# Kernel tuning notes

Hardware: AMD Instinct MI355X
Metric: run time of the kernel (lower is better)

The kernel has to match this reference:

```python
import jax, jax.numpy as jnp
import numpy as np

D_MODEL = 512
NHEAD = 8
D_K = D_MODEL // NHEAD


def setup_inputs() -> dict:
    key = jax.random.key(0)
    ks = jax.random.split(key, 7)
    B, L = 4, 2048
    x = jax.random.normal(ks[0], (B, L, D_MODEL), dtype=jnp.float32)
    scale = 1.0 / np.sqrt(D_MODEL)
    Wq = jax.random.normal(ks[1], (D_MODEL, D_MODEL), dtype=jnp.float32) * scale
    Wk = jax.random.normal(ks[2], (D_MODEL, D_MODEL), dtype=jnp.float32) * scale
    Wv = jax.random.normal(ks[3], (D_MODEL, D_MODEL), dtype=jnp.float32) * scale
    Wo = jax.random.normal(ks[4], (D_MODEL, D_MODEL), dtype=jnp.float32) * scale
    wave_freq = jax.random.normal(ks[5], (NHEAD,), dtype=jnp.float32) * 0.1
    wave_phase = jnp.zeros((NHEAD,), dtype=jnp.float32)
    return {"x": x, "Wq": Wq, "Wk": Wk, "Wv": Wv, "Wo": Wo,
            "wave_freq": wave_freq, "wave_phase": wave_phase}


def reference(x, Wq, Wk, Wv, Wo, wave_freq, wave_phase):
    B, L, D = x.shape
    H, dk = NHEAD, D_K
    # nn.Linear(bias=False): y = x @ W.T
    q = (x @ Wq.T).reshape(B, L, H, dk).transpose(0, 2, 1, 3)  # (B,H,L,dk)
    k = (x @ Wk.T).reshape(B, L, H, dk).transpose(0, 2, 1, 3)
    v = (x @ Wv.T).reshape(B, L, H, dk).transpose(0, 2, 1, 3)
    pos = jnp.arange(L, dtype=x.dtype)  # (L,)
    two_pi = jnp.asarray(2.0 * np.pi, dtype=x.dtype)
    # wave: (H, L) -> broadcast as (1, H, 1, L) over key positions
    wave = jnp.cos(two_pi * wave_freq[:, None] * pos[None, :] + wave_phase[:, None])
    scores = jnp.einsum('bhqd,bhkd->bhqk', q, k) * (dk ** -0.5)
    scores = scores * wave[None, :, None, :]
    attn = jax.nn.softmax(scores, axis=-1)
    out = jnp.einsum('bhqk,bhkd->bhqd', attn, v)
    out = out.transpose(0, 2, 1, 3).reshape(B, L, D)
    return out @ Wo.T
```

## Files before the change

kernel.cpp:

```cpp
#include <hip/hip_runtime.h>
#include <math.h>

#define D_MODEL 512
#define NHEAD   8
#define DK      64
#define BATCH   4
#define SEQ     2048
#define MTOT    (BATCH*SEQ)
#define NXELEM  (MTOT*D_MODEL)
#define NWELEM  (4*D_MODEL*D_MODEL)

typedef _Float16 half8   __attribute__((ext_vector_type(8)));
typedef _Float16 half4_t __attribute__((ext_vector_type(4)));
typedef __fp16   fp16x2  __attribute__((ext_vector_type(2)));
typedef float    f32x4   __attribute__((ext_vector_type(4)));

#define MFMA32(a,b,c) __builtin_amdgcn_mfma_f32_16x16x32_f16((a),(b),(c),0,0,0)

#define WSCALE 0.18033688011117130f

__global__ __launch_bounds__(256) void cvt_kernel(
    const float* __restrict__ x,
    const float* __restrict__ Wq, const float* __restrict__ Wk,
    const float* __restrict__ Wv, const float* __restrict__ Wo,
    const float* __restrict__ wf, const float* __restrict__ wp,
    _Float16* __restrict__ Xh, _Float16* __restrict__ Wh,
    float* __restrict__ wtab)
{
    const int tid = blockIdx.x * 256 + threadIdx.x;
    int idx = tid * 4;
    if (idx < NXELEM + NWELEM) {
        const float* src; _Float16* dst; int off;
        if (idx < NXELEM) { src = x; dst = Xh; off = idx; }
        else {
            int r = idx - NXELEM;
            int sel = r >> 18;
            off = r & ((1 << 18) - 1);
            src = (sel == 0) ? Wq : (sel == 1) ? Wk : (sel == 2) ? Wv : Wo;
            dst = Wh + ((size_t)sel << 18);
        }
        float4 v = *(const float4*)(src + off);
        half4_t h;
        h[0] = (_Float16)v.x; h[1] = (_Float16)v.y;
        h[2] = (_Float16)v.z; h[3] = (_Float16)v.w;
        *(half4_t*)(dst + off) = h;
    } else {
        int widx = idx - (NXELEM + NWELEM);
        const int h = widx >> 11;
        const int pos0 = widx & 2047;
        const float f  = 6.28318530717958647692f * wf[h];
        const float ph = wp[h];
        float4 o;
        o.x = WSCALE * cosf(fmaf(f, (float)(pos0 + 0), ph));
        o.y = WSCALE * cosf(fmaf(f, (float)(pos0 + 1), ph));
        o.z = WSCALE * cosf(fmaf(f, (float)(pos0 + 2), ph));
        o.w = WSCALE * cosf(fmaf(f, (float)(pos0 + 3), ph));
        *(float4*)(wtab + widx) = o;
    }
}

__global__ __launch_bounds__(256) void qkv_mfma_kernel(
    const _Float16* __restrict__ Xh, const _Float16* __restrict__ Wh,
    const float* __restrict__ wtab,
    _Float16* __restrict__ Qh, _Float16* __restrict__ Kh,
    _Float16* __restrict__ Vth)
{
    __shared__ _Float16 As[128][72];
    __shared__ _Float16 Bs[64][72];

    const int t  = threadIdx.x;
    const int n0 = blockIdx.x * 64;
    const int m0 = blockIdx.y * 128;
    const int which = n0 >> 9;
    const int h = (n0 >> 6) & 7;
    const _Float16* Wbase = Wh + ((size_t)which << 18) + (size_t)(h * 64) * 512;

    const int w = t >> 6, lane = t & 63, ln = lane & 15, quad = lane >> 4;
    const int ar = t >> 1, ac = (t & 1) * 32;
    const int br = t >> 2, bc = (t & 3) * 16;

    const _Float16* ag = Xh + (size_t)(m0 + ar) * 512 + ac;
    const _Float16* bg = Wbase + (size_t)br * 512 + bc;

    const f32x4 kZero = {0.f, 0.f, 0.f, 0.f};
    f32x4 acc[2][4];
    #pragma unroll
    for (int i = 0; i < 2; ++i)
        #pragma unroll
        for (int j = 0; j < 4; ++j) acc[i][j] = kZero;

    for (int k0 = 0; k0 < 512; k0 += 64) {
        half8 av[4], bv[2];
        #pragma unroll
        for (int i = 0; i < 4; ++i) av[i] = *(const half8*)(ag + k0 + i * 8);
        #pragma unroll
        for (int i = 0; i < 2; ++i) bv[i] = *(const half8*)(bg + k0 + i * 8);
        __syncthreads();
        #pragma unroll
        for (int i = 0; i < 4; ++i) *(half8*)&As[ar][ac + i * 8] = av[i];
        #pragma unroll
        for (int i = 0; i < 2; ++i) *(half8*)&Bs[br][bc + i * 8] = bv[i];
        __syncthreads();

        #pragma unroll
        for (int ks = 0; ks < 2; ++ks) {
            half8 af[2], bf[4];
            #pragma unroll
            for (int mt = 0; mt < 2; ++mt)
                af[mt] = *(const half8*)&As[w * 32 + mt * 16 + ln][ks * 32 + quad * 8];
            #pragma unroll
            for (int nt = 0; nt < 4; ++nt)
                bf[nt] = *(const half8*)&Bs[nt * 16 + ln][ks * 32 + quad * 8];
            #pragma unroll
            for (int mt = 0; mt < 2; ++mt)
                #pragma unroll
                for (int nt = 0; nt < 4; ++nt)
                    acc[mt][nt] = MFMA32(af[mt], bf[nt], acc[mt][nt]);
        }
    }

    const int b  = m0 >> 11;
    const int l0 = m0 & 2047;

    if (which < 2) {
        _Float16* dst = (which == 0 ? Qh : Kh) + (size_t)(b * NHEAD + h) * SEQ * DK;
        const float* wt = wtab + h * SEQ;
        __syncthreads();
        _Float16* Ql = &As[0][0];
        #pragma unroll
        for (int mt = 0; mt < 2; ++mt)
            #pragma unroll
            for (int r = 0; r < 4; ++r) {
                const int lr = w * 32 + mt * 16 + quad * 4 + r;
                const float wv = (which == 1) ? wt[l0 + lr] : 1.0f;
                #pragma unroll
                for (int nt = 0; nt < 4; ++nt)
                    Ql[lr * 72 + nt * 16 + ln] = (_Float16)(acc[mt][nt][r] * wv);
            }
        __syncthreads();
        #pragma unroll
        for (int rr = 0; rr < 4; ++rr) {
            const int row = rr * 32 + (t >> 3);
            half8 v = *(const half8*)&Ql[row * 72 + (t & 7) * 8];
            *(half8*)(dst + (size_t)(l0 + row) * DK + (t & 7) * 8) = v;
        }
    } else {
        __syncthreads();
        _Float16* Vl = &As[0][0];
        #pragma unroll
        for (int nt = 0; nt < 4; ++nt) {
            half8 hv;
            #pragma unroll
            for (int mt = 0; mt < 2; ++mt)
                #pragma unroll
                for (int r = 0; r < 4; ++r)
                    hv[mt * 4 + r] = (_Float16)acc[mt][nt][r];
            const int d = nt * 16 + ln;
            *(half8*)&Vl[d * 136 + w * 32 + quad * 8] = hv;
        }
        __syncthreads();
        _Float16* dst = Vth + (size_t)(b * NHEAD + h) * DK * SEQ;
        #pragma unroll
        for (int rr = 0; rr < 4; ++rr) {
            const int d = rr * 16 + (t >> 4);
            half8 v = *(const half8*)&Vl[d * 136 + (t & 15) * 8];
            *(half8*)(dst + (size_t)d * SEQ + l0 + (t & 15) * 8) = v;
        }
    }
}

__global__ __launch_bounds__(256) void attn_mfma_kernel(
    const _Float16* __restrict__ Qh, const _Float16* __restrict__ Kwh,
    const _Float16* __restrict__ Vth, _Float16* __restrict__ AOh)
{
    __shared__ _Float16 SM[4][64][72];

    const int bx = blockIdx.x;
    const int g8 = bx & 7;
    const int s  = bx >> 3;
    const int bh = g8 * 4 + (s >> 4);
    const int q0 = (s & 15) * 128;
    const int b = bh >> 3, h = bh & 7;

    const int t = threadIdx.x;
    const int w = t >> 6, lane = t & 63, ln = lane & 15, quad = lane >> 4;

    const _Float16* Qg = Qh + ((size_t)bh * SEQ + q0) * DK;
    const _Float16* Kg = Kwh + (size_t)bh * SEQ * DK;
    const _Float16* Vg = Vth + (size_t)bh * DK * SEQ;

    const int sr = t >> 2, sc = (t & 3) * 16;
    const int qr = t >> 1, qc = (t & 1) * 32;

    {
        const _Float16* qp = Qg + (size_t)qr * DK + qc;
        half8 qv0 = *(const half8*)(qp);
        half8 qv1 = *(const half8*)(qp + 8);
        half8 qv2 = *(const half8*)(qp + 16);
        half8 qv3 = *(const half8*)(qp + 24);
        const _Float16* kp = Kg + (size_t)sr * DK + sc;
        const _Float16* vp = Vg + (size_t)sr * SEQ + sc;
        half8 kv0 = *(const half8*)(kp);
        half8 kv1 = *(const half8*)(kp + 8);
        half8 vv0 = *(const half8*)(vp);
        half8 vv1 = *(const half8*)(vp + 8);
        _Float16* qd = &SM[2 + (qr >> 6)][qr & 63][qc];
        *(half8*)(qd)      = qv0;
        *(half8*)(qd + 8)  = qv1;
        *(half8*)(qd + 16) = qv2;
        *(half8*)(qd + 24) = qv3;
        *(half8*)&SM[0][sr][sc]     = kv0;
        *(half8*)&SM[0][sr][sc + 8] = kv1;
        *(half8*)&SM[1][sr][sc]     = vv0;
        *(half8*)&SM[1][sr][sc + 8] = vv1;
    }
    __syncthreads();

    half8 qf[2][2];
    #pragma unroll
    for (int u = 0; u < 2; ++u) {
        const int row = w * 32 + u * 16 + ln;
        const _Float16* qsrc = &SM[2 + (row >> 6)][row & 63][0];
        qf[u][0] = *(const half8*)(qsrc + quad * 8);
        qf[u][1] = *(const half8*)(qsrc + 32 + quad * 8);
    }
    __syncthreads();

    const f32x4 kZero = {0.f, 0.f, 0.f, 0.f};
    f32x4 o[2][4];
    #pragma unroll
    for (int u = 0; u < 2; ++u)
        #pragma unroll
        for (int nt = 0; nt < 4; ++nt) o[u][nt] = kZero;
    float l_acc[2] = {0.f, 0.f};

    for (int kt = 0; kt < SEQ / 64; ++kt) {
        const int cur = kt & 1;

        half8 pk0, pk1, pv0, pv1;
        const bool more = (kt + 1 < SEQ / 64);
        if (more) {
            const _Float16* kp = Kg + (size_t)((kt + 1) * 64 + sr) * DK + sc;
            const _Float16* vp = Vg + (size_t)sr * SEQ + (kt + 1) * 64 + sc;
            pk0 = *(const half8*)(kp);
            pk1 = *(const half8*)(kp + 8);
            pv0 = *(const half8*)(vp);
            pv1 = *(const half8*)(vp + 8);
        }

        const _Float16 (*Ks)[72] = SM[2 * cur];
        const _Float16 (*Vs)[72] = SM[2 * cur + 1];

        #pragma unroll
        for (int g = 0; g < 2; ++g) {
            half8 ka0 = *(const half8*)&Ks[(2 * g + 0) * 16 + ln][quad * 8];
            half8 ka1 = *(const half8*)&Ks[(2 * g + 0) * 16 + ln][32 + quad * 8];
            half8 kb0 = *(const half8*)&Ks[(2 * g + 1) * 16 + ln][quad * 8];
            half8 kb1 = *(const half8*)&Ks[(2 * g + 1) * 16 + ln][32 + quad * 8];
            half8 vf[4];
            #pragma unroll
            for (int nt = 0; nt < 4; ++nt)
                vf[nt] = *(const half8*)&Vs[nt * 16 + ln][g * 32 + quad * 8];

            #pragma unroll
            for (int u = 0; u < 2; ++u) {
                f32x4 s0 = MFMA32(ka0, qf[u][0], kZero);
                f32x4 s1 = MFMA32(kb0, qf[u][0], kZero);
                s0 = MFMA32(ka1, qf[u][1], s0);
                s1 = MFMA32(kb1, qf[u][1], s1);

                const float e00 = __builtin_amdgcn_exp2f(s0[0]);
                const float e01 = __builtin_amdgcn_exp2f(s0[1]);
                const float e02 = __builtin_amdgcn_exp2f(s0[2]);
                const float e03 = __builtin_amdgcn_exp2f(s0[3]);
                const float e10 = __builtin_amdgcn_exp2f(s1[0]);
                const float e11 = __builtin_amdgcn_exp2f(s1[1]);
                const float e12 = __builtin_amdgcn_exp2f(s1[2]);
                const float e13 = __builtin_amdgcn_exp2f(s1[3]);
                union { half8 v; fp16x2 h2[4]; } pu;
                pu.h2[0] = __builtin_amdgcn_cvt_pkrtz(e00, e01);
                pu.h2[1] = __builtin_amdgcn_cvt_pkrtz(e02, e03);
                pu.h2[2] = __builtin_amdgcn_cvt_pkrtz(e10, e11);
                pu.h2[3] = __builtin_amdgcn_cvt_pkrtz(e12, e13);
                l_acc[u] += ((e00 + e01) + (e02 + e03)) + ((e10 + e11) + (e12 + e13));

                #pragma unroll
                for (int nt = 0; nt < 4; ++nt)
                    o[u][nt] = MFMA32(pu.v, vf[nt], o[u][nt]);
            }
        }

        __syncthreads();
        if (more) {
            _Float16* kd = &SM[2 * (cur ^ 1)][sr][sc];
            _Float16* vd = &SM[2 * (cur ^ 1) + 1][sr][sc];
            *(half8*)(kd)     = pk0;
            *(half8*)(kd + 8) = pk1;
            *(half8*)(vd)     = pv0;
            *(half8*)(vd + 8) = pv1;
        }
        __syncthreads();
    }

    #pragma unroll
    for (int u = 0; u < 2; ++u) {
        l_acc[u] += __shfl_xor(l_acc[u], 16);
        l_acc[u] += __shfl_xor(l_acc[u], 32);
    }

    #pragma unroll
    for (int u = 0; u < 2; ++u)
        #pragma unroll
        for (int r = 0; r < 4; ++r) {
            const float lr  = __shfl(l_acc[u], quad * 4 + r, 16);
            const float inv = 1.0f / lr;
            const int lq = q0 + w * 32 + u * 16 + quad * 4 + r;
            const size_t base = ((size_t)b * SEQ + lq) * D_MODEL + h * DK;
            #pragma unroll
            for (int nt = 0; nt < 4; ++nt)
                AOh[base + nt * 16 + ln] = (_Float16)(o[u][nt][r] * inv);
        }
}

__global__ __launch_bounds__(256) void out_mfma_kernel(
    const _Float16* __restrict__ AOh, const _Float16* __restrict__ Woh,
    float* __restrict__ out)
{
    __shared__ _Float16 As[128][72];
    __shared__ _Float16 Bs[64][72];

    const int t  = threadIdx.x;
    const int n0 = blockIdx.x * 64;
    const int m0 = blockIdx.y * 128;

    const int w = t >> 6, lane = t & 63, ln = lane & 15, quad = lane >> 4;
    const int ar = t >> 1, ac = (t & 1) * 32;
    const int br = t >> 2, bc = (t & 3) * 16;

    const _Float16* ag = AOh + (size_t)(m0 + ar) * 512 + ac;
    const _Float16* bg = Woh + (size_t)(n0 + br) * 512 + bc;

    const f32x4 kZero = {0.f, 0.f, 0.f, 0.f};
    f32x4 acc[2][4];
    #pragma unroll
    for (int i = 0; i < 2; ++i)
        #pragma unroll
        for (int j = 0; j < 4; ++j) acc[i][j] = kZero;

    for (int k0 = 0; k0 < 512; k0 += 64) {
        half8 av[4], bv[2];
        #pragma unroll
        for (int i = 0; i < 4; ++i) av[i] = *(const half8*)(ag + k0 + i * 8);
        #pragma unroll
        for (int i = 0; i < 2; ++i) bv[i] = *(const half8*)(bg + k0 + i * 8);
        __syncthreads();
        #pragma unroll
        for (int i = 0; i < 4; ++i) *(half8*)&As[ar][ac + i * 8] = av[i];
        #pragma unroll
        for (int i = 0; i < 2; ++i) *(half8*)&Bs[br][bc + i * 8] = bv[i];
        __syncthreads();

        #pragma unroll
        for (int ks = 0; ks < 2; ++ks) {
            half8 af[2], bf[4];
            #pragma unroll
            for (int mt = 0; mt < 2; ++mt)
                af[mt] = *(const half8*)&As[w * 32 + mt * 16 + ln][ks * 32 + quad * 8];
            #pragma unroll
            for (int nt = 0; nt < 4; ++nt)
                bf[nt] = *(const half8*)&Bs[nt * 16 + ln][ks * 32 + quad * 8];
            #pragma unroll
            for (int mt = 0; mt < 2; ++mt)
                #pragma unroll
                for (int nt = 0; nt < 4; ++nt)
                    acc[mt][nt] = MFMA32(af[mt], bf[nt], acc[mt][nt]);
        }
    }

    float* Os = (float*)&As[0][0];
    #pragma unroll
    for (int pass = 0; pass < 2; ++pass) {
        __syncthreads();
        if ((w >> 1) == pass) {
            const int rbase = (w & 1) * 32;
            #pragma unroll
            for (int mt = 0; mt < 2; ++mt)
                #pragma unroll
                for (int r = 0; r < 4; ++r) {
                    const int row = rbase + mt * 16 + quad * 4 + r;
                    #pragma unroll
                    for (int nt = 0; nt < 4; ++nt)
                        Os[row * 66 + nt * 16 + ln] = acc[mt][nt][r];
                }
        }
        __syncthreads();
        #pragma unroll
        for (int rr = 0; rr < 4; ++rr) {
            const int row = rr * 16 + (t >> 4);
            float4 v = *(const float4*)&Os[row * 66 + (t & 15) * 4];
            *(float4*)(out + (size_t)(m0 + pass * 64 + row) * 512 + n0 + (t & 15) * 4) = v;
        }
    }
}

extern "C" void kernel_launch(void* const* d_in, const int* in_sizes, int n_in,
                              void* d_out, int out_size, void* d_ws, size_t ws_size,
                              hipStream_t stream)
{
    (void)in_sizes; (void)n_in; (void)out_size; (void)ws_size;
    const float* x  = (const float*)d_in[0];
    const float* Wq = (const float*)d_in[1];
    const float* Wk = (const float*)d_in[2];
    const float* Wv = (const float*)d_in[3];
    const float* Wo = (const float*)d_in[4];
    const float* wf = (const float*)d_in[5];
    const float* wp = (const float*)d_in[6];
    float* out = (float*)d_out;

    const size_t NX = (size_t)MTOT * D_MODEL;
    _Float16* Xh  = (_Float16*)d_ws;
    _Float16* Wh  = Xh + NX;
    _Float16* Qh  = Wh + 4 * 262144;
    _Float16* Kh  = Qh + NX;
    _Float16* Vth = Kh + NX;
    _Float16* AOh = Vth + NX;
    float*    wtab = (float*)(AOh + NX);

    cvt_kernel<<<5136, 256, 0, stream>>>(x, Wq, Wk, Wv, Wo, wf, wp, Xh, Wh, wtab);

    dim3 g1(24, 64);
    qkv_mfma_kernel<<<g1, 256, 0, stream>>>(Xh, Wh, wtab, Qh, Kh, Vth);

    attn_mfma_kernel<<<512, 256, 0, stream>>>(Qh, Kh, Vth, AOh);

    dim3 g3(8, 64);
    out_mfma_kernel<<<g3, 256, 0, stream>>>(AOh, Wh + 3 * 262144, out);
}
```

Baseline: 167.2 us.

## Fuse Q/K/V projections per head and split attention keys across two wave groups

```diff
diff --git a/kernel.cpp b/kernel.cpp
--- a/kernel.cpp
+++ b/kernel.cpp
@@ -66,65 +66,78 @@
     _Float16* __restrict__ Vth)
 {
     __shared__ _Float16 As[128][72];
-    __shared__ _Float16 Bs[64][72];
+    __shared__ _Float16 Bs[192][72];
 
     const int t  = threadIdx.x;
-    const int n0 = blockIdx.x * 64;
+    const int h  = blockIdx.x;
     const int m0 = blockIdx.y * 128;
-    const int which = n0 >> 9;
-    const int h = (n0 >> 6) & 7;
-    const _Float16* Wbase = Wh + ((size_t)which << 18) + (size_t)(h * 64) * 512;
 
     const int w = t >> 6, lane = t & 63, ln = lane & 15, quad = lane >> 4;
     const int ar = t >> 1, ac = (t & 1) * 32;
     const int br = t >> 2, bc = (t & 3) * 16;
 
-    const _Float16* ag = Xh + (size_t)(m0 + ar) * 512 + ac;
-    const _Float16* bg = Wbase + (size_t)br * 512 + bc;
+    const _Float16* ag  = Xh + (size_t)(m0 + ar) * 512 + ac;
+    const _Float16* bg0 = Wh + (size_t)(h * 64 + br) * 512 + bc;
+    const _Float16* bg1 = bg0 + (1 << 18);
+    const _Float16* bg2 = bg0 + (2 << 18);
 
     const f32x4 kZero = {0.f, 0.f, 0.f, 0.f};
-    f32x4 acc[2][4];
-    #pragma unroll
-    for (int i = 0; i < 2; ++i)
-        #pragma unroll
-        for (int j = 0; j < 4; ++j) acc[i][j] = kZero;
+    f32x4 acc[3][2][4];
+    #pragma unroll
+    for (int c = 0; c < 3; ++c)
+        #pragma unroll
+        for (int i = 0; i < 2; ++i)
+            #pragma unroll
+            for (int j = 0; j < 4; ++j) acc[c][i][j] = kZero;
 
     for (int k0 = 0; k0 < 512; k0 += 64) {
-        half8 av[4], bv[2];
+        half8 av[4], bv[6];
         #pragma unroll
         for (int i = 0; i < 4; ++i) av[i] = *(const half8*)(ag + k0 + i * 8);
-        #pragma unroll
-        for (int i = 0; i < 2; ++i) bv[i] = *(const half8*)(bg + k0 + i * 8);
+        bv[0] = *(const half8*)(bg0 + k0);
+        bv[1] = *(const half8*)(bg0 + k0 + 8);
+        bv[2] = *(const half8*)(bg1 + k0);
+        bv[3] = *(const half8*)(bg1 + k0 + 8);
+        bv[4] = *(const half8*)(bg2 + k0);
+        bv[5] = *(const half8*)(bg2 + k0 + 8);
         __syncthreads();
         #pragma unroll
         for (int i = 0; i < 4; ++i) *(half8*)&As[ar][ac + i * 8] = av[i];
         #pragma unroll
-        for (int i = 0; i < 2; ++i) *(half8*)&Bs[br][bc + i * 8] = bv[i];
+        for (int c = 0; c < 3; ++c) {
+            *(half8*)&Bs[c * 64 + br][bc]     = bv[2 * c];
+            *(half8*)&Bs[c * 64 + br][bc + 8] = bv[2 * c + 1];
+        }
         __syncthreads();
 
         #pragma unroll
         for (int ks = 0; ks < 2; ++ks) {
-            half8 af[2], bf[4];
+            half8 af[2];
             #pragma unroll
             for (int mt = 0; mt < 2; ++mt)
                 af[mt] = *(const half8*)&As[w * 32 + mt * 16 + ln][ks * 32 + quad * 8];
             #pragma unroll
-            for (int nt = 0; nt < 4; ++nt)
-                bf[nt] = *(const half8*)&Bs[nt * 16 + ln][ks * 32 + quad * 8];
-            #pragma unroll
-            for (int mt = 0; mt < 2; ++mt)
+            for (int c = 0; c < 3; ++c) {
+                half8 bf[4];
                 #pragma unroll
                 for (int nt = 0; nt < 4; ++nt)
-                    acc[mt][nt] = MFMA32(af[mt], bf[nt], acc[mt][nt]);
+                    bf[nt] = *(const half8*)&Bs[c * 64 + nt * 16 + ln][ks * 32 + quad * 8];
+                #pragma unroll
+                for (int mt = 0; mt < 2; ++mt)
+                    #pragma unroll
+                    for (int nt = 0; nt < 4; ++nt)
+                        acc[c][mt][nt] = MFMA32(af[mt], bf[nt], acc[c][mt][nt]);
+            }
         }
     }
 
     const int b  = m0 >> 11;
     const int l0 = m0 & 2047;
-
-    if (which < 2) {
+    const float* wt = wtab + h * SEQ;
+
+    #pragma unroll
+    for (int which = 0; which < 2; ++which) {
         _Float16* dst = (which == 0 ? Qh : Kh) + (size_t)(b * NHEAD + h) * SEQ * DK;
-        const float* wt = wtab + h * SEQ;
         __syncthreads();
         _Float16* Ql = &As[0][0];
         #pragma unroll
@@ -135,7 +148,7 @@
                 const float wv = (which == 1) ? wt[l0 + lr] : 1.0f;
                 #pragma unroll
                 for (int nt = 0; nt < 4; ++nt)
-                    Ql[lr * 72 + nt * 16 + ln] = (_Float16)(acc[mt][nt][r] * wv);
+                    Ql[lr * 72 + nt * 16 + ln] = (_Float16)(acc[which][mt][nt][r] * wv);
             }
         __syncthreads();
         #pragma unroll
@@ -144,36 +157,36 @@
             half8 v = *(const half8*)&Ql[row * 72 + (t & 7) * 8];
             *(half8*)(dst + (size_t)(l0 + row) * DK + (t & 7) * 8) = v;
         }
-    } else {
-        __syncthreads();
-        _Float16* Vl = &As[0][0];
-        #pragma unroll
-        for (int nt = 0; nt < 4; ++nt) {
-            half8 hv;
-            #pragma unroll
-            for (int mt = 0; mt < 2; ++mt)
-                #pragma unroll
-                for (int r = 0; r < 4; ++r)
-                    hv[mt * 4 + r] = (_Float16)acc[mt][nt][r];
-            const int d = nt * 16 + ln;
-            *(half8*)&Vl[d * 136 + w * 32 + quad * 8] = hv;
-        }
-        __syncthreads();
-        _Float16* dst = Vth + (size_t)(b * NHEAD + h) * DK * SEQ;
-        #pragma unroll
-        for (int rr = 0; rr < 4; ++rr) {
-            const int d = rr * 16 + (t >> 4);
-            half8 v = *(const half8*)&Vl[d * 136 + (t & 15) * 8];
-            *(half8*)(dst + (size_t)d * SEQ + l0 + (t & 15) * 8) = v;
-        }
+    }
+
+    __syncthreads();
+    _Float16* Vl = &As[0][0];
+    #pragma unroll
+    for (int nt = 0; nt < 4; ++nt) {
+        half8 hv;
+        #pragma unroll
+        for (int mt = 0; mt < 2; ++mt)
+            #pragma unroll
+            for (int r = 0; r < 4; ++r)
+                hv[mt * 4 + r] = (_Float16)acc[2][mt][nt][r];
+        const int d = nt * 16 + ln;
+        *(half8*)&Vl[d * 136 + w * 32 + quad * 8] = hv;
+    }
+    __syncthreads();
+    _Float16* dst = Vth + (size_t)(b * NHEAD + h) * DK * SEQ;
+    #pragma unroll
+    for (int rr = 0; rr < 4; ++rr) {
+        const int d = rr * 16 + (t >> 4);
+        half8 v = *(const half8*)&Vl[d * 136 + (t & 15) * 8];
+        *(half8*)(dst + (size_t)d * SEQ + l0 + (t & 15) * 8) = v;
     }
 }
 
-__global__ __launch_bounds__(256) void attn_mfma_kernel(
+__global__ __launch_bounds__(512, 4) void attn_mfma_kernel(
     const _Float16* __restrict__ Qh, const _Float16* __restrict__ Kwh,
     const _Float16* __restrict__ Vth, _Float16* __restrict__ AOh)
 {
-    __shared__ _Float16 SM[4][64][72];
+    __shared__ _Float16 SM[2][4][64][72];
 
     const int bx = blockIdx.x;
     const int g8 = bx & 7;
@@ -183,48 +196,48 @@
     const int b = bh >> 3, h = bh & 7;
 
     const int t = threadIdx.x;
-    const int w = t >> 6, lane = t & 63, ln = lane & 15, quad = lane >> 4;
+    const int w = t >> 6;
+    const int wg = w & 3;
+    const int half = w >> 2;
+    const int lane = t & 63, ln = lane & 15, quad = lane >> 4;
 
     const _Float16* Qg = Qh + ((size_t)bh * SEQ + q0) * DK;
     const _Float16* Kg = Kwh + (size_t)bh * SEQ * DK;
     const _Float16* Vg = Vth + (size_t)bh * DK * SEQ;
-
-    const int sr = t >> 2, sc = (t & 3) * 16;
-    const int qr = t >> 1, qc = (t & 1) * 32;
+    const int kbase = half * 1024;
+
+    const int tl = t & 255;
+    const int sr = tl >> 2, sc = (tl & 3) * 16;
+    const int qr = t >> 2, qc = (t & 3) * 16;
 
     {
         const _Float16* qp = Qg + (size_t)qr * DK + qc;
         half8 qv0 = *(const half8*)(qp);
         half8 qv1 = *(const half8*)(qp + 8);
-        half8 qv2 = *(const half8*)(qp + 16);
-        half8 qv3 = *(const half8*)(qp + 24);
-        const _Float16* kp = Kg + (size_t)sr * DK + sc;
-        const _Float16* vp = Vg + (size_t)sr * SEQ + sc;
+        const _Float16* kp = Kg + (size_t)(kbase + sr) * DK + sc;
+        const _Float16* vp = Vg + (size_t)sr * SEQ + kbase + sc;
         half8 kv0 = *(const half8*)(kp);
         half8 kv1 = *(const half8*)(kp + 8);
         half8 vv0 = *(const half8*)(vp);
         half8 vv1 = *(const half8*)(vp + 8);
-        _Float16* qd = &SM[2 + (qr >> 6)][qr & 63][qc];
-        *(half8*)(qd)      = qv0;
-        *(half8*)(qd + 8)  = qv1;
-        *(half8*)(qd + 16) = qv2;
-        *(half8*)(qd + 24) = qv3;
-        *(half8*)&SM[0][sr][sc]     = kv0;
-        *(half8*)&SM[0][sr][sc + 8] = kv1;
-        *(half8*)&SM[1][sr][sc]     = vv0;
-        *(half8*)&SM[1][sr][sc + 8] = vv1;
+        _Float16* qd = &SM[1][2 + (qr >> 6)][qr & 63][qc];
+        *(half8*)(qd)     = qv0;
+        *(half8*)(qd + 8) = qv1;
+        *(half8*)&SM[half][0][sr][sc]     = kv0;
+        *(half8*)&SM[half][0][sr][sc + 8] = kv1;
+        *(half8*)&SM[half][1][sr][sc]     = vv0;
+        *(half8*)&SM[half][1][sr][sc + 8] = vv1;
     }
     __syncthreads();
 
     half8 qf[2][2];
     #pragma unroll
     for (int u = 0; u < 2; ++u) {
-        const int row = w * 32 + u * 16 + ln;
-        const _Float16* qsrc = &SM[2 + (row >> 6)][row & 63][0];
+        const int row = wg * 32 + u * 16 + ln;
+        const _Float16* qsrc = &SM[1][2 + (row >> 6)][row & 63][0];
         qf[u][0] = *(const half8*)(qsrc + quad * 8);
         qf[u][1] = *(const half8*)(qsrc + 32 + quad * 8);
     }
-    __syncthreads();
 
     const f32x4 kZero = {0.f, 0.f, 0.f, 0.f};
     f32x4 o[2][4];
@@ -234,22 +247,22 @@
         for (int nt = 0; nt < 4; ++nt) o[u][nt] = kZero;
     float l_acc[2] = {0.f, 0.f};
 
-    for (int kt = 0; kt < SEQ / 64; ++kt) {
+    for (int kt = 0; kt < 16; ++kt) {
         const int cur = kt & 1;
 
         half8 pk0, pk1, pv0, pv1;
-        const bool more = (kt + 1 < SEQ / 64);
+        const bool more = (kt + 1 < 16);
         if (more) {
-            const _Float16* kp = Kg + (size_t)((kt + 1) * 64 + sr) * DK + sc;
-            const _Float16* vp = Vg + (size_t)sr * SEQ + (kt + 1) * 64 + sc;
+            const _Float16* kp = Kg + (size_t)(kbase + (kt + 1) * 64 + sr) * DK + sc;
+            const _Float16* vp = Vg + (size_t)sr * SEQ + kbase + (kt + 1) * 64 + sc;
             pk0 = *(const half8*)(kp);
             pk1 = *(const half8*)(kp + 8);
             pv0 = *(const half8*)(vp);
             pv1 = *(const half8*)(vp + 8);
         }
 
-        const _Float16 (*Ks)[72] = SM[2 * cur];
-        const _Float16 (*Vs)[72] = SM[2 * cur + 1];
+        const _Float16 (*Ks)[72] = SM[half][2 * cur];
+        const _Float16 (*Vs)[72] = SM[half][2 * cur + 1];
 
         #pragma unroll
         for (int g = 0; g < 2; ++g) {
@@ -292,8 +305,8 @@
 
         __syncthreads();
         if (more) {
-            _Float16* kd = &SM[2 * (cur ^ 1)][sr][sc];
-            _Float16* vd = &SM[2 * (cur ^ 1) + 1][sr][sc];
+            _Float16* kd = &SM[half][2 * (cur ^ 1)][sr][sc];
+            _Float16* vd = &SM[half][2 * (cur ^ 1) + 1][sr][sc];
             *(half8*)(kd)     = pk0;
             *(half8*)(kd + 8) = pk1;
             *(half8*)(vd)     = pv0;
@@ -302,24 +315,50 @@
         __syncthreads();
     }
 
-    #pragma unroll
-    for (int u = 0; u < 2; ++u) {
-        l_acc[u] += __shfl_xor(l_acc[u], 16);
-        l_acc[u] += __shfl_xor(l_acc[u], 32);
-    }
-
-    #pragma unroll
-    for (int u = 0; u < 2; ++u)
-        #pragma unroll
-        for (int r = 0; r < 4; ++r) {
-            const float lr  = __shfl(l_acc[u], quad * 4 + r, 16);
-            const float inv = 1.0f / lr;
-            const int lq = q0 + w * 32 + u * 16 + quad * 4 + r;
-            const size_t base = ((size_t)b * SEQ + lq) * D_MODEL + h * DK;
+    float* OP = (float*)&SM[0][0][0][0];
+    const int idx = wg * 64 + lane;
+    if (half == 1) {
+        #pragma unroll
+        for (int u = 0; u < 2; ++u)
             #pragma unroll
             for (int nt = 0; nt < 4; ++nt)
-                AOh[base + nt * 16 + ln] = (_Float16)(o[u][nt][r] * inv);
-        }
+                #pragma unroll
+                for (int r = 0; r < 4; ++r)
+                    OP[((u * 4 + nt) * 4 + r) * 257 + idx] = o[u][nt][r];
+        OP[32 * 257 + idx] = l_acc[0];
+        OP[33 * 257 + idx] = l_acc[1];
+    }
+    __syncthreads();
+    if (half == 0) {
+        #pragma unroll
+        for (int u = 0; u < 2; ++u)
+            #pragma unroll
+            for (int nt = 0; nt < 4; ++nt)
+                #pragma unroll
+                for (int r = 0; r < 4; ++r)
+                    o[u][nt][r] += OP[((u * 4 + nt) * 4 + r) * 257 + idx];
+        l_acc[0] += OP[32 * 257 + idx];
+        l_acc[1] += OP[33 * 257 + idx];
+
+        #pragma unroll
+        for (int u = 0; u < 2; ++u) {
+            l_acc[u] += __shfl_xor(l_acc[u], 16);
+            l_acc[u] += __shfl_xor(l_acc[u], 32);
+        }
+
+        #pragma unroll
+        for (int u = 0; u < 2; ++u)
+            #pragma unroll
+            for (int r = 0; r < 4; ++r) {
+                const float lr  = __shfl(l_acc[u], quad * 4 + r, 16);
+                const float inv = 1.0f / lr;
+                const int lq = q0 + wg * 32 + u * 16 + quad * 4 + r;
+                const size_t base = ((size_t)b * SEQ + lq) * D_MODEL + h * DK;
+                #pragma unroll
+                for (int nt = 0; nt < 4; ++nt)
+                    AOh[base + nt * 16 + ln] = (_Float16)(o[u][nt][r] * inv);
+            }
+    }
 }
 
 __global__ __launch_bounds__(256) void out_mfma_kernel(
@@ -428,10 +467,10 @@
 
     cvt_kernel<<<5136, 256, 0, stream>>>(x, Wq, Wk, Wv, Wo, wf, wp, Xh, Wh, wtab);
 
-    dim3 g1(24, 64);
+    dim3 g1(8, 64);
     qkv_mfma_kernel<<<g1, 256, 0, stream>>>(Xh, Wh, wtab, Qh, Kh, Vth);
 
-    attn_mfma_kernel<<<512, 256, 0, stream>>>(Qh, Kh, Vth, AOh);
+    attn_mfma_kernel<<<512, 512, 0, stream>>>(Qh, Kh, Vth, AOh);
 
     dim3 g3(8, 64);
     out_mfma_kernel<<<g3, 256, 0, stream>>>(AOh, Wh + 3 * 262144, out);
```

New measurement: 155.7 us. -6.8%, faster.
